# Performance work log

Hardware: AMD Instinct MI355X
Metric: run time of the kernel (lower is better)

Reference implementation:

```python
import jax, jax.numpy as jnp
import numpy as np

DIM = 768
HEADS = 12
HEAD_DIM = DIM // HEADS
SCALE = HEAD_DIM ** -0.5


def setup_inputs() -> dict:
    key = jax.random.key(0)
    ks = jax.random.split(key, 6)
    B, N = 4, 2048
    x = jax.random.normal(ks[0], (B, N, DIM), dtype=jnp.float32)
    s = DIM ** -0.5
    Wq = jax.random.normal(ks[1], (DIM, DIM), dtype=jnp.float32) * s
    Wk = jax.random.normal(ks[2], (DIM, DIM), dtype=jnp.float32) * s
    Wv = jax.random.normal(ks[3], (DIM, DIM), dtype=jnp.float32) * s
    Wp = jax.random.normal(ks[4], (DIM, DIM), dtype=jnp.float32) * s
    bp = jnp.zeros((DIM,), dtype=jnp.float32)
    return {"x": x, "Wq": Wq, "Wk": Wk, "Wv": Wv, "Wp": Wp, "bp": bp}


def reference(x, Wq, Wk, Wv, Wp, bp):
    B, N, C = x.shape
    # separate Q/K/V linears (no bias, qkv_bias=False); torch Linear: x @ W.T
    q = (x @ Wq.T).reshape(B, N, HEADS, HEAD_DIM).transpose(0, 2, 1, 3)
    k = (x @ Wk.T).reshape(B, N, HEADS, HEAD_DIM).transpose(0, 2, 1, 3)
    v = (x @ Wv.T).reshape(B, N, HEADS, HEAD_DIM).transpose(0, 2, 1, 3)
    # explicit full [B,H,N,N] attention matrix, as in the source
    attn = jnp.einsum("bhqd,bhkd->bhqk", q, k) * SCALE
    attn = jax.nn.softmax(attn, axis=-1)
    out = jnp.einsum("bhqk,bhkd->bhqd", attn, v)
    out = out.transpose(0, 2, 1, 3).reshape(B, N, C)
    return out @ Wp.T + bp
```

## Files before the change

### kernel.cpp

```cpp
#include <hip/hip_runtime.h>
#include <cstdint>

#define DIM   768
#define HEADS 12
#define HDIM  64
#define BATCH 4
#define SEQ   2048
#define MROWS (BATCH*SEQ)

typedef __bf16 bf16;
typedef __bf16 bf16x4_t __attribute__((ext_vector_type(4)));
typedef __bf16 bf16x8_t __attribute__((ext_vector_type(8)));
typedef float  f32x4_t  __attribute__((ext_vector_type(4)));
typedef short  short4_t __attribute__((ext_vector_type(4)));

__device__ __forceinline__ f32x4_t mfma16x16x16bf16(bf16x4_t a, bf16x4_t b, f32x4_t c) {
#if __has_builtin(__builtin_amdgcn_mfma_f32_16x16x16_bf16)
    return __builtin_amdgcn_mfma_f32_16x16x16_bf16(a, b, c, 0, 0, 0);
#elif __has_builtin(__builtin_amdgcn_mfma_f32_16x16x16bf16_1k)
    union U { bf16x4_t h; short4_t s; };
    U ua, ub; ua.h = a; ub.h = b;
    return __builtin_amdgcn_mfma_f32_16x16x16bf16_1k(ua.s, ub.s, c, 0, 0, 0);
#else
    asm("v_mfma_f32_16x16x16_bf16 %0, %1, %2, %0" : "+v"(c) : "v"(a), "v"(b));
    return c;
#endif
}

__global__ void cast_bf16_kernel(const float* __restrict__ src, bf16* __restrict__ dst, int n4) {
    int i = blockIdx.x * blockDim.x + threadIdx.x;
    if (i >= n4) return;
    const float4 v = reinterpret_cast<const float4*>(src)[i];
    bf16x4_t o;
    o[0] = (bf16)v.x; o[1] = (bf16)v.y; o[2] = (bf16)v.z; o[3] = (bf16)v.w;
    reinterpret_cast<bf16x4_t*>(dst)[i] = o;
}

__global__ void cast_w4_kernel(const float* __restrict__ s0, const float* __restrict__ s1,
                               const float* __restrict__ s2, const float* __restrict__ s3,
                               bf16* __restrict__ d0, bf16* __restrict__ d1,
                               bf16* __restrict__ d2, bf16* __restrict__ d3, int n4) {
    int i = blockIdx.x * blockDim.x + threadIdx.x;
    if (i >= n4) return;
    int y = blockIdx.y;
    const float* src = (y == 0) ? s0 : (y == 1) ? s1 : (y == 2) ? s2 : s3;
    bf16* dst        = (y == 0) ? d0 : (y == 1) ? d1 : (y == 2) ? d2 : d3;
    const float4 v = reinterpret_cast<const float4*>(src)[i];
    bf16x4_t o;
    o[0] = (bf16)v.x; o[1] = (bf16)v.y; o[2] = (bf16)v.z; o[3] = (bf16)v.w;
    reinterpret_cast<bf16x4_t*>(dst)[i] = o;
}

__device__ __forceinline__ void gload_lds16(const bf16* g, bf16* l) {
    __builtin_amdgcn_global_load_lds((const __attribute__((address_space(1))) void*)g,
                                     (__attribute__((address_space(3))) void*)l, 16, 0, 0);
}

__global__ __launch_bounds__(256, 2) void qkv_gemm(
        const bf16* __restrict__ X,
        const bf16* __restrict__ Wq, const bf16* __restrict__ Wk,
        bf16* __restrict__ Q, bf16* __restrict__ Kd)
{
    __shared__ bf16 As[128*32];
    __shared__ bf16 Bs[128*32];
    const int tid  = threadIdx.x;
    const int z    = blockIdx.z;
    const bf16* W  = (z == 0) ? Wq : Wk;
    const int n0   = blockIdx.x * 128;
    const int m0   = blockIdx.y * 128;
    const int lane = tid & 63;
    const int w    = tid >> 6;
    const int wm   = (w & 1) * 64, wn = (w >> 1) * 64;
    const int lr   = lane & 15, quad = lane >> 4;

    f32x4_t acc[4][4] = {};

    for (int kk = 0; kk < DIM; kk += 32) {
        #pragma unroll
        for (int i = 0; i < 2; ++i) {
            int c = tid + i * 256;
            int row = c >> 2, ko = (c & 3) * 8;
            gload_lds16(X + (size_t)(m0 + row) * DIM + kk + ko, &As[row * 32 + ko]);
            gload_lds16(W + (size_t)(n0 + row) * DIM + kk + ko, &Bs[row * 32 + ko]);
        }
        __syncthreads();
        bf16x8_t af[4], bfr[4];
        #pragma unroll
        for (int i = 0; i < 4; ++i)
            af[i] = *reinterpret_cast<const bf16x8_t*>(&As[(wm + i * 16 + lr) * 32 + quad * 8]);
        #pragma unroll
        for (int j = 0; j < 4; ++j)
            bfr[j] = *reinterpret_cast<const bf16x8_t*>(&Bs[(wn + j * 16 + lr) * 32 + quad * 8]);
        #pragma unroll
        for (int i = 0; i < 4; ++i)
            #pragma unroll
            for (int j = 0; j < 4; ++j)
                acc[i][j] = __builtin_amdgcn_mfma_f32_16x16x32_bf16(af[i], bfr[j], acc[i][j], 0, 0, 0);
        __syncthreads();
    }

    const float sc = (z == 0) ? 0.18033688011112042f : 1.0f;
    bf16* dst = (z == 0) ? Q : Kd;
    #pragma unroll
    for (int i = 0; i < 4; ++i) {
        int mbase = m0 + wm + i * 16 + quad * 4;
        #pragma unroll
        for (int j = 0; j < 4; ++j) {
            int n = n0 + wn + j * 16 + lr;
            int h = n >> 6, d = n & 63;
            #pragma unroll
            for (int r = 0; r < 4; ++r) {
                int m = mbase + r;
                int b = m >> 11, row = m & 2047;
                dst[(((size_t)b * HEADS + h) * SEQ + row) * HDIM + d] = (bf16)(acc[i][j][r] * sc);
            }
        }
    }
}

__global__ __launch_bounds__(256, 2) void vt_gemm(
        const bf16* __restrict__ Wv,
        const bf16* __restrict__ X,
        bf16* __restrict__ Vt)
{
    __shared__ bf16 As[128*32];
    __shared__ bf16 Bs[128*32];
    const int tid  = threadIdx.x;
    const int n0   = blockIdx.x * 128;
    const int m0   = blockIdx.y * 128;
    const int lane = tid & 63;
    const int w    = tid >> 6;
    const int wm   = (w & 1) * 64, wn = (w >> 1) * 64;
    const int lr   = lane & 15, quad = lane >> 4;

    f32x4_t acc[4][4] = {};

    for (int kk = 0; kk < DIM; kk += 32) {
        #pragma unroll
        for (int i = 0; i < 2; ++i) {
            int c = tid + i * 256;
            int row = c >> 2, ko = (c & 3) * 8;
            gload_lds16(Wv + (size_t)(m0 + row) * DIM + kk + ko, &As[row * 32 + ko]);
            gload_lds16(X  + (size_t)(n0 + row) * DIM + kk + ko, &Bs[row * 32 + ko]);
        }
        __syncthreads();
        bf16x8_t af[4], bfr[4];
        #pragma unroll
        for (int i = 0; i < 4; ++i)
            af[i] = *reinterpret_cast<const bf16x8_t*>(&As[(wm + i * 16 + lr) * 32 + quad * 8]);
        #pragma unroll
        for (int j = 0; j < 4; ++j)
            bfr[j] = *reinterpret_cast<const bf16x8_t*>(&Bs[(wn + j * 16 + lr) * 32 + quad * 8]);
        #pragma unroll
        for (int i = 0; i < 4; ++i)
            #pragma unroll
            for (int j = 0; j < 4; ++j)
                acc[i][j] = __builtin_amdgcn_mfma_f32_16x16x32_bf16(af[i], bfr[j], acc[i][j], 0, 0, 0);
        __syncthreads();
    }

    #pragma unroll
    for (int i = 0; i < 4; ++i) {
        int mbase = m0 + wm + i * 16 + quad * 4;
        #pragma unroll
        for (int j = 0; j < 4; ++j) {
            int n = n0 + wn + j * 16 + lr;
            #pragma unroll
            for (int r = 0; r < 4; ++r)
                Vt[(size_t)(mbase + r) * MROWS + n] = (bf16)acc[i][j][r];
        }
    }
}

__global__ __launch_bounds__(256, 2) void out_gemm(
        const bf16* __restrict__ A,
        const bf16* __restrict__ W,
        const float* __restrict__ bias,
        float* __restrict__ out)
{
    __shared__ bf16 As[128*32];
    __shared__ bf16 Bs[128*32];
    const int tid  = threadIdx.x;
    const int n0   = blockIdx.x * 128;
    const int m0   = blockIdx.y * 128;
    const int lane = tid & 63;
    const int w    = tid >> 6;
    const int wm   = (w & 1) * 64, wn = (w >> 1) * 64;
    const int lr   = lane & 15, quad = lane >> 4;

    f32x4_t acc[4][4] = {};

    for (int kk = 0; kk < DIM; kk += 32) {
        #pragma unroll
        for (int i = 0; i < 2; ++i) {
            int c = tid + i * 256;
            int row = c >> 2, ko = (c & 3) * 8;
            gload_lds16(A + (size_t)(m0 + row) * DIM + kk + ko, &As[row * 32 + ko]);
            gload_lds16(W + (size_t)(n0 + row) * DIM + kk + ko, &Bs[row * 32 + ko]);
        }
        __syncthreads();
        bf16x8_t af[4], bfr[4];
        #pragma unroll
        for (int i = 0; i < 4; ++i)
            af[i] = *reinterpret_cast<const bf16x8_t*>(&As[(wm + i * 16 + lr) * 32 + quad * 8]);
        #pragma unroll
        for (int j = 0; j < 4; ++j)
            bfr[j] = *reinterpret_cast<const bf16x8_t*>(&Bs[(wn + j * 16 + lr) * 32 + quad * 8]);
        #pragma unroll
        for (int i = 0; i < 4; ++i)
            #pragma unroll
            for (int j = 0; j < 4; ++j)
                acc[i][j] = __builtin_amdgcn_mfma_f32_16x16x32_bf16(af[i], bfr[j], acc[i][j], 0, 0, 0);
        __syncthreads();
    }

    #pragma unroll
    for (int i = 0; i < 4; ++i) {
        int mbase = m0 + wm + i * 16 + quad * 4;
        #pragma unroll
        for (int j = 0; j < 4; ++j) {
            int n = n0 + wn + j * 16 + lr;
            float bv = bias[n];
            #pragma unroll
            for (int r = 0; r < 4; ++r) {
                int m = mbase + r;
                out[(size_t)m * DIM + n] = acc[i][j][r] + bv;
            }
        }
    }
}

__global__ __launch_bounds__(256, 4) void attn_kernel(
        const bf16* __restrict__ Q, const bf16* __restrict__ Kd,
        const bf16* __restrict__ Vt, bf16* __restrict__ Ab)
{
    __shared__ __align__(16) bf16 KV[2][2][64*64];

    const int tid  = threadIdx.x;
    const int bh   = blockIdx.y;
    const int b    = bh / HEADS, h = bh % HEADS;
    const int q0   = blockIdx.x * 128;
    const int lane = tid & 63, w = tid >> 6;
    const int lr   = lane & 15, quad = lane >> 4;
    const int wq   = w * 32;

    const size_t qkbase = (size_t)bh * SEQ * HDIM;
    const size_t vbase  = (size_t)h * HDIM * MROWS + (size_t)b * SEQ;

    const int src_row = tid >> 3, src_ch = tid & 7;
    const int src_gch = src_ch ^ (src_row & 7);
    const int src_row2 = (tid + 256) >> 3, src_ch2 = tid & 7;
    const int src_gch2 = src_ch2 ^ (src_row2 & 7);

    {
        bf16* Qst = &KV[1][0][0];
        #pragma unroll
        for (int i = 0; i < 4; ++i) {
            int c = tid + i * 256;
            int row = c >> 3, ch = c & 7;
            int gch = ch ^ (row & 7);
            gload_lds16(Q + qkbase + (size_t)(q0 + row) * HDIM + gch * 8, &Qst[row * 64 + ch * 8]);
        }
    }

    const bf16* kp1 = Kd + qkbase + (size_t)src_row  * HDIM + src_gch  * 8;
    const bf16* kp2 = Kd + qkbase + (size_t)src_row2 * HDIM + src_gch2 * 8;
    const bf16* vp1 = Vt + vbase  + (size_t)src_row  * MROWS + src_gch  * 8;
    const bf16* vp2 = Vt + vbase  + (size_t)src_row2 * MROWS + src_gch2 * 8;
    bf16* kl1 = &KV[0][0][src_row  * 64 + src_ch  * 8];
    bf16* kl2 = &KV[0][0][src_row2 * 64 + src_ch2 * 8];
    bf16* vl1 = &KV[0][1][src_row  * 64 + src_ch  * 8];
    bf16* vl2 = &KV[0][1][src_row2 * 64 + src_ch2 * 8];
    const ptrdiff_t kstep = 64 * HDIM, vstep = 64;
    const ptrdiff_t lstep = 2 * 64 * 64;

    gload_lds16(kp1, kl1); gload_lds16(kp2, kl2);
    gload_lds16(vp1, vl1); gload_lds16(vp2, vl2);
    __syncthreads();

    bf16x8_t qf[2][2];
    {
        const bf16* Qst = &KV[1][0][0];
        #pragma unroll
        for (int q16 = 0; q16 < 2; ++q16) {
            int row = wq + q16 * 16 + lr;
            #pragma unroll
            for (int ks = 0; ks < 2; ++ks) {
                int ch = (ks * 4 + quad) ^ (row & 7);
                qf[q16][ks] = *reinterpret_cast<const bf16x8_t*>(&Qst[row * 64 + ch * 8]);
            }
        }
    }
    __syncthreads();

    f32x4_t oacc[2][4] = {};
    f32x4_t rsacc[2] = {};
    bf16x4_t ones4;
    ones4[0] = (bf16)1.0f; ones4[1] = (bf16)1.0f; ones4[2] = (bf16)1.0f; ones4[3] = (bf16)1.0f;

    for (int it = 0; it < SEQ / 64; ++it) {
        const int buf = it & 1;
        if (it + 1 < SEQ / 64) {
            const ptrdiff_t g = (ptrdiff_t)(it + 1);
            const ptrdiff_t l = (buf ^ 1) ? lstep : 0;
            gload_lds16(kp1 + g * kstep, kl1 + l); gload_lds16(kp2 + g * kstep, kl2 + l);
            gload_lds16(vp1 + g * vstep, vl1 + l); gload_lds16(vp2 + g * vstep, vl2 + l);
        }

        const bf16* Ks = &KV[buf][0][0];
        const bf16* Vs = &KV[buf][1][0];

        f32x4_t sacc[4][2] = {};
        #pragma unroll
        for (int ks = 0; ks < 2; ++ks) {
            bf16x8_t af[4];
            #pragma unroll
            for (int kt = 0; kt < 4; ++kt) {
                int row = kt * 16 + lr;
                int ch = (ks * 4 + quad) ^ (row & 7);
                af[kt] = *reinterpret_cast<const bf16x8_t*>(&Ks[row * 64 + ch * 8]);
            }
            #pragma unroll
            for (int kt = 0; kt < 4; ++kt)
                #pragma unroll
                for (int q16 = 0; q16 < 2; ++q16)
                    sacc[kt][q16] = __builtin_amdgcn_mfma_f32_16x16x32_bf16(
                        af[kt], qf[q16][ks], sacc[kt][q16], 0, 0, 0);
        }

        #pragma unroll
        for (int kt = 0; kt < 4; ++kt) {
            bf16x4_t bv[4];
            #pragma unroll
            for (int dt = 0; dt < 4; ++dt) {
                int row = dt * 16 + lr;
                int ch = (2 * kt + (quad >> 1)) ^ (row & 7);
                bv[dt] = *reinterpret_cast<const bf16x4_t*>(&Vs[row * 64 + ch * 8 + (quad & 1) * 4]);
            }
            #pragma unroll
            for (int q16 = 0; q16 < 2; ++q16) {
                bf16x4_t pk;
                #pragma unroll
                for (int r = 0; r < 4; ++r)
                    pk[r] = (bf16)__builtin_amdgcn_exp2f(sacc[kt][q16][r]);
                rsacc[q16] = mfma16x16x16bf16(pk, ones4, rsacc[q16]);
                #pragma unroll
                for (int dt = 0; dt < 4; ++dt)
                    oacc[q16][dt] = mfma16x16x16bf16(pk, bv[dt], oacc[q16][dt]);
            }
        }
        __syncthreads();
    }

    #pragma unroll
    for (int q16 = 0; q16 < 2; ++q16) {
        float inv[4];
        #pragma unroll
        for (int r = 0; r < 4; ++r)
            inv[r] = 1.0f / rsacc[q16][r];
        #pragma unroll
        for (int dt = 0; dt < 4; ++dt) {
            #pragma unroll
            for (int r = 0; r < 4; ++r) {
                int q = q0 + wq + q16 * 16 + quad * 4 + r;
                Ab[((size_t)b * SEQ + q) * DIM + h * HDIM + dt * 16 + lr] =
                    (bf16)(oacc[q16][dt][r] * inv[r]);
            }
        }
    }
}

extern "C" void kernel_launch(void* const* d_in, const int* in_sizes, int n_in,
                              void* d_out, int out_size, void* d_ws, size_t ws_size,
                              hipStream_t stream) {
    (void)in_sizes; (void)n_in; (void)out_size; (void)ws_size;
    const float* x  = (const float*)d_in[0];
    const float* Wq = (const float*)d_in[1];
    const float* Wk = (const float*)d_in[2];
    const float* Wv = (const float*)d_in[3];
    const float* Wp = (const float*)d_in[4];
    const float* bp = (const float*)d_in[5];
    float* out = (float*)d_out;

    char* ws = (char*)d_ws;
    size_t off = 0;
    auto alloc = [&](size_t bytes) {
        void* p = ws + off;
        off += (bytes + 255) & ~(size_t)255;
        return p;
    };
    const size_t big = (size_t)MROWS * DIM * sizeof(bf16);
    const size_t wsz = (size_t)DIM * DIM * sizeof(bf16);
    bf16* Xb  = (bf16*)alloc(big);
    bf16* Qb  = (bf16*)alloc(big);
    bf16* Kb  = (bf16*)alloc(big);
    bf16* Vtb = (bf16*)alloc(big);
    bf16* Wqb = (bf16*)alloc(wsz);
    bf16* Wkb = (bf16*)alloc(wsz);
    bf16* Wvb = (bf16*)alloc(wsz);
    bf16* Wpb = (bf16*)alloc(wsz);
    bf16* Ab  = Xb;

    const int x4 = MROWS * DIM / 4;
    cast_bf16_kernel<<<(x4 + 255) / 256, 256, 0, stream>>>(x, Xb, x4);
    const int w4 = DIM * DIM / 4;
    cast_w4_kernel<<<dim3((w4 + 255) / 256, 4), 256, 0, stream>>>(
        Wq, Wk, Wv, Wp, Wqb, Wkb, Wvb, Wpb, w4);

    qkv_gemm<<<dim3(DIM / 128, MROWS / 128, 2), 256, 0, stream>>>(Xb, Wqb, Wkb, Qb, Kb);
    vt_gemm<<<dim3(MROWS / 128, DIM / 128), 256, 0, stream>>>(Wvb, Xb, Vtb);

    attn_kernel<<<dim3(SEQ / 128, BATCH * HEADS), 256, 0, stream>>>(Qb, Kb, Vtb, Ab);

    out_gemm<<<dim3(DIM / 128, MROWS / 128), 256, 0, stream>>>(Ab, Wpb, bp, out);
}
```

Baseline: 234.1 us.

## Shrink attention query tile to 64 rows per block for more parallelism

Each attention block now handles 64 queries instead of 128, with every wave owning one 16-row query tile rather than two, and the grid doubles in the sequence dimension. The aim is more blocks and lower register pressure per wave, so more blocks can stay resident and the GPU is better filled (the launch bound is raised to 5). The cost is that every K/V tile loaded into shared memory is reused by half as many queries, which doubles global K/V traffic and the LDS loads per MFMA.

Measured after the change: 241.5 us. 3.2% more time.

```diff
diff --git a/kernel.cpp b/kernel.cpp
--- a/kernel.cpp
+++ b/kernel.cpp
@@ -230,7 +230,7 @@
     }
 }
 
-__global__ __launch_bounds__(256, 4) void attn_kernel(
+__global__ __launch_bounds__(256, 5) void attn_kernel(
         const bf16* __restrict__ Q, const bf16* __restrict__ Kd,
         const bf16* __restrict__ Vt, bf16* __restrict__ Ab)
 {
@@ -239,10 +239,10 @@
     const int tid  = threadIdx.x;
     const int bh   = blockIdx.y;
     const int b    = bh / HEADS, h = bh % HEADS;
-    const int q0   = blockIdx.x * 128;
+    const int q0   = blockIdx.x * 64;
     const int lane = tid & 63, w = tid >> 6;
     const int lr   = lane & 15, quad = lane >> 4;
-    const int wq   = w * 32;
+    const int wq   = w * 16;
 
     const size_t qkbase = (size_t)bh * SEQ * HDIM;
     const size_t vbase  = (size_t)h * HDIM * MROWS + (size_t)b * SEQ;
@@ -254,13 +254,10 @@
 
     {
         bf16* Qst = &KV[1][0][0];
-        #pragma unroll
-        for (int i = 0; i < 4; ++i) {
-            int c = tid + i * 256;
-            int row = c >> 3, ch = c & 7;
-            int gch = ch ^ (row & 7);
-            gload_lds16(Q + qkbase + (size_t)(q0 + row) * HDIM + gch * 8, &Qst[row * 64 + ch * 8]);
-        }
+        gload_lds16(Q + qkbase + (size_t)(q0 + src_row) * HDIM + src_gch * 8,
+                    &Qst[src_row * 64 + src_ch * 8]);
+        gload_lds16(Q + qkbase + (size_t)(q0 + src_row2) * HDIM + src_gch2 * 8,
+                    &Qst[src_row2 * 64 + src_ch2 * 8]);
     }
 
     const bf16* kp1 = Kd + qkbase + (size_t)src_row  * HDIM + src_gch  * 8;
@@ -278,23 +275,20 @@
     gload_lds16(vp1, vl1); gload_lds16(vp2, vl2);
     __syncthreads();
 
-    bf16x8_t qf[2][2];
+    bf16x8_t qf[2];
     {
         const bf16* Qst = &KV[1][0][0];
-        #pragma unroll
-        for (int q16 = 0; q16 < 2; ++q16) {
-            int row = wq + q16 * 16 + lr;
-            #pragma unroll
-            for (int ks = 0; ks < 2; ++ks) {
-                int ch = (ks * 4 + quad) ^ (row & 7);
-                qf[q16][ks] = *reinterpret_cast<const bf16x8_t*>(&Qst[row * 64 + ch * 8]);
-            }
+        int row = wq + lr;
+        #pragma unroll
+        for (int ks = 0; ks < 2; ++ks) {
+            int ch = (ks * 4 + quad) ^ (row & 7);
+            qf[ks] = *reinterpret_cast<const bf16x8_t*>(&Qst[row * 64 + ch * 8]);
         }
     }
     __syncthreads();
 
-    f32x4_t oacc[2][4] = {};
-    f32x4_t rsacc[2] = {};
+    f32x4_t oacc[4] = {};
+    f32x4_t rsacc = {};
     bf16x4_t ones4;
     ones4[0] = (bf16)1.0f; ones4[1] = (bf16)1.0f; ones4[2] = (bf16)1.0f; ones4[3] = (bf16)1.0f;
 
@@ -310,7 +304,7 @@
         const bf16* Ks = &KV[buf][0][0];
         const bf16* Vs = &KV[buf][1][0];
 
-        f32x4_t sacc[4][2] = {};
+        f32x4_t sacc[4] = {};
         #pragma unroll
         for (int ks = 0; ks < 2; ++ks) {
             bf16x8_t af[4];
@@ -322,10 +316,8 @@
             }
             #pragma unroll
             for (int kt = 0; kt < 4; ++kt)
-                #pragma unroll
-                for (int q16 = 0; q16 < 2; ++q16)
-                    sacc[kt][q16] = __builtin_amdgcn_mfma_f32_16x16x32_bf16(
-                        af[kt], qf[q16][ks], sacc[kt][q16], 0, 0, 0);
+                sacc[kt] = __builtin_amdgcn_mfma_f32_16x16x32_bf16(
+                    af[kt], qf[ks], sacc[kt], 0, 0, 0);
         }
 
         #pragma unroll
@@ -337,35 +329,29 @@
                 int ch = (2 * kt + (quad >> 1)) ^ (row & 7);
                 bv[dt] = *reinterpret_cast<const bf16x4_t*>(&Vs[row * 64 + ch * 8 + (quad & 1) * 4]);
             }
-            #pragma unroll
-            for (int q16 = 0; q16 < 2; ++q16) {
-                bf16x4_t pk;
-                #pragma unroll
-                for (int r = 0; r < 4; ++r)
-                    pk[r] = (bf16)__builtin_amdgcn_exp2f(sacc[kt][q16][r]);
-                rsacc[q16] = mfma16x16x16bf16(pk, ones4, rsacc[q16]);
-                #pragma unroll
-                for (int dt = 0; dt < 4; ++dt)
-                    oacc[q16][dt] = mfma16x16x16bf16(pk, bv[dt], oacc[q16][dt]);
-            }
-        }
-        __syncthreads();
-    }
-
+            bf16x4_t pk;
+            #pragma unroll
+            for (int r = 0; r < 4; ++r)
+                pk[r] = (bf16)__builtin_amdgcn_exp2f(sacc[kt][r]);
+            rsacc = mfma16x16x16bf16(pk, ones4, rsacc);
+            #pragma unroll
+            for (int dt = 0; dt < 4; ++dt)
+                oacc[dt] = mfma16x16x16bf16(pk, bv[dt], oacc[dt]);
+        }
+        __syncthreads();
+    }
+
+    float inv[4];
     #pragma unroll
-    for (int q16 = 0; q16 < 2; ++q16) {
-        float inv[4];
-        #pragma unroll
-        for (int r = 0; r < 4; ++r)
-            inv[r] = 1.0f / rsacc[q16][r];
-        #pragma unroll
-        for (int dt = 0; dt < 4; ++dt) {
-            #pragma unroll
-            for (int r = 0; r < 4; ++r) {
-                int q = q0 + wq + q16 * 16 + quad * 4 + r;
-                Ab[((size_t)b * SEQ + q) * DIM + h * HDIM + dt * 16 + lr] =
-                    (bf16)(oacc[q16][dt][r] * inv[r]);
-            }
+    for (int r = 0; r < 4; ++r)
+        inv[r] = 1.0f / rsacc[r];
+    #pragma unroll
+    for (int dt = 0; dt < 4; ++dt) {
+        #pragma unroll
+        for (int r = 0; r < 4; ++r) {
+            int q = q0 + wq + quad * 4 + r;
+            Ab[((size_t)b * SEQ + q) * DIM + h * HDIM + dt * 16 + lr] =
+                (bf16)(oacc[dt][r] * inv[r]);
         }
     }
 }
@@ -410,7 +396,7 @@
     qkv_gemm<<<dim3(DIM / 128, MROWS / 128, 2), 256, 0, stream>>>(Xb, Wqb, Wkb, Qb, Kb);
     vt_gemm<<<dim3(MROWS / 128, DIM / 128), 256, 0, stream>>>(Wvb, Xb, Vtb);
 
-    attn_kernel<<<dim3(SEQ / 128, BATCH * HEADS), 256, 0, stream>>>(Qb, Kb, Vtb, Ab);
+    attn_kernel<<<dim3(SEQ / 64, BATCH * HEADS), 256, 0, stream>>>(Qb, Kb, Vtb, Ab);
 
     out_gemm<<<dim3(DIM / 128, MROWS / 128), 256, 0, stream>>>(Ab, Wpb, bp, out);
 }
```
